# Kernel tuning notes

Hardware: AMD Instinct MI355X
Metric: run time of the kernel (lower is better)

## Reference

```python
import jax, jax.numpy as jnp
import numpy as np

B, L, HID = 512, 128, 384
N_LABELS, N_SLOTS = 32, 128


def setup_inputs() -> dict:
    key = jax.random.key(0)
    ks = jax.random.split(key, 16)

    def g(k, shape, scale):
        return jax.random.normal(k, shape, dtype=jnp.float32) * scale

    sent_lens = jax.random.randint(ks[0], (B,), 1, L + 1)
    mask = (jnp.arange(L)[None, :] < sent_lens[:, None]).astype(jnp.float32)[..., None]
    # zero out padded token positions to mimic the ragged original
    H = g(ks[1], (B, L, HID), 1.0) * mask
    c_slot_cont = g(ks[2], (B, L, HID), 1.0) * mask
    c_inte = g(ks[3], (B, HID), 1.0)
    s = 1.0 / np.sqrt(HID)
    return {
        "H": H,
        "c_slot_cont": c_slot_cont,
        "c_inte": c_inte,
        "W0": g(ks[4], (HID, HID), s),
        "W1": g(ks[5], (HID, HID), s),
        "W2": g(ks[6], (HID, HID), s),
        "W3": g(ks[7], (HID, HID), s),
        "W4": g(ks[8], (HID, HID), s),
        "b4": g(ks[9], (HID,), s),
        "W5": g(ks[10], (HID, 1), s),
        "V_SF": g(ks[11], (HID, HID), s),
        "W_inte": g(ks[12], (HID, N_LABELS), s),
        "W_slot": g(ks[13], (2 * HID, N_SLOTS), s),
        "sent_lens": sent_lens,
        "iteration_num": 3,
    }


def reference(H, c_slot_cont, c_inte, W0, W1, W2, W3, W4, b4, W5, V_SF,
              W_inte, W_slot, sent_lens, iteration_num):
    Ld = H.shape[1]
    mask = jnp.arange(Ld)[None, :] < sent_lens[:, None]          # [B, L] bool
    maskf = mask[..., None].astype(H.dtype)                       # [B, L, 1]
    neg_inf = jnp.finfo(H.dtype).min

    def sf_fusion(x, y):
        # SF_FusionLayer (dropout off / eval); inner loop runs once since nth=2
        x0 = jnp.tanh(x)
        y0 = jnp.tanh(y)
        f = jax.nn.sigmoid(jnp.tanh(x0 @ W0 + y0 @ W1) @ W2)
        x2 = f * x0 + x
        y2 = (1.0 - f) * y0 + y
        return f * x2 + (1.0 - f) * y2

    def id_fusion(x, y):
        # ID_FusionLayer; softmax over token dim, masked per sentence
        x0 = jnp.tanh(x)
        y0 = jnp.tanh(y)
        rates = ((x @ W3 + y @ W4 + b4) @ W5)[..., 0]             # [B, L]
        rates = jnp.where(mask, rates, neg_inf)
        alphas = jax.nn.softmax(rates, axis=1)[..., None]         # [B, L, 1]
        x2 = alphas * x0 + x
        y2 = (1.0 - alphas) * y0 + y
        return alphas * x2 + (1.0 - alphas) * y2

    r_inte = c_inte                                               # [B, HID]
    r_slot = c_slot_cont
    for _ in range(iteration_num):
        f_slot = sf_fusion(c_slot_cont, r_inte[:, None, :])       # [B, L, HID]
        f_slot = jnp.sum((f_slot @ V_SF) * maskf, axis=1)         # [B, HID]
        r_slot = f_slot[:, None, :] * c_slot_cont                 # [B, L, HID]
        f_inte = jnp.sum(id_fusion(r_slot, H) * maskf, axis=1)    # [B, HID]
        r_inte = f_inte + c_inte

    intent_output = r_inte @ W_inte                               # [B, n_labels]
    slot_output = jnp.concatenate([H, r_slot], axis=-1) @ W_slot  # [B, L, n_slots]
    return intent_output, slot_output
```

## Files before the change

### kernel.cpp

```cpp
#include <hip/hip_runtime.h>
#include <math.h>

#define HID 384
#define SLEN 128
#define NB 512
#define MTOK (NB*SLEN)
#define NLAB 32
#define NSLOT 128
#define APITCH 40
#define GPITCH 72

typedef _Float16 h8 __attribute__((ext_vector_type(8)));
typedef _Float16 h4v __attribute__((ext_vector_type(4)));
typedef __bf16   b8 __attribute__((ext_vector_type(8)));
typedef float    f4 __attribute__((ext_vector_type(4)));

__device__ __forceinline__ float sane(float x){
  return __builtin_isfinite(x) ? x : 0.f;
}
__device__ __forceinline__ float clampf(float x, float lo, float hi){
  return fminf(hi, fmaxf(lo, x));
}
__device__ __forceinline__ float fast_rcp(float x){
  return __builtin_amdgcn_rcpf(x);
}
__device__ __forceinline__ float fast_tanh(float x){
  x = clampf(x, -15.f, 15.f);
  float e = __expf(2.f * x);
  return (e - 1.f) * fast_rcp(e + 1.f);
}
__device__ __forceinline__ float sigmoid_c(float x){
  x = clampf(x, -60.f, 60.f);
  return fast_rcp(1.f + __expf(-x));
}
__device__ __forceinline__ void split16(float x, _Float16* h, _Float16* l){
  _Float16 hh = (_Float16)x; *h = hh; *l = (_Float16)(x - (float)hh);
}
__device__ __forceinline__ h8 ldh(const _Float16* p){ return *reinterpret_cast<const h8*>(p); }
__device__ __forceinline__ b8 ldb(const __bf16* p){ return *reinterpret_cast<const b8*>(p); }
__device__ __forceinline__ f4 mfma16h(h8 a, h8 b, f4 c){
  return __builtin_amdgcn_mfma_f32_16x16x32_f16(a, b, c, 0, 0, 0);
}
__device__ __forceinline__ f4 mfma16b(b8 a, b8 b, f4 c){
  return __builtin_amdgcn_mfma_f32_16x16x32_bf16(a, b, c, 0, 0, 0);
}


__global__ void k_lens(const int* __restrict__ raw, int* __restrict__ lensN){
  const int b = threadIdx.x;
  __shared__ int is64;
  if (b == 0) is64 = (raw[1] == 0) ? 1 : 0;
  __syncthreads();
  int v = is64 ? raw[2 * b] : raw[b];
  v = v < 0 ? 0 : (v > SLEN ? SLEN : v);
  lensN[b] = v;
}

__global__ void k_wsplit16(const float* __restrict__ in, _Float16* __restrict__ outh,
                           _Float16* __restrict__ outl, int R, int C){
  int idx = blockIdx.x * blockDim.x + threadIdx.x;
  if (idx < R * C){
    int r = idx / C, c = idx - r * C;
    float v = sane(in[idx]);
    _Float16 h = (_Float16)v;
    outh[(size_t)c * R + r] = h;
    outl[(size_t)c * R + r] = (_Float16)(v - (float)h);
  }
}

__global__ void k_wsplitbf(const float* __restrict__ in, __bf16* __restrict__ outh,
                           __bf16* __restrict__ outl, int R, int C){
  int idx = blockIdx.x * blockDim.x + threadIdx.x;
  if (idx < R * C){
    int r = idx / C, c = idx - r * C;
    float v = sane(in[idx]);
    __bf16 h = (__bf16)v;
    outh[(size_t)c * R + r] = h;
    outl[(size_t)c * R + r] = (__bf16)(v - (float)h);
  }
}

__global__ void k_transpose32(const float* __restrict__ in, float* __restrict__ out,
                              int R, int C){
  int idx = blockIdx.x * blockDim.x + threadIdx.x;
  if (idx < R * C){ int r = idx / C, c = idx - r * C; out[(size_t)c * R + r] = sane(in[idx]); }
}

__global__ void k_sanecopy(const float* __restrict__ in, float* __restrict__ out, int n){
  int i = blockIdx.x * blockDim.x + threadIdx.x;
  if (i < n) out[i] = sane(in[i]);
}

__global__ void k_w35(const float* __restrict__ W3, const float* __restrict__ W4,
                      const float* __restrict__ b4, const float* __restrict__ W5,
                      float* __restrict__ w35, float* __restrict__ w45, float* __restrict__ b45){
  __shared__ float w5s[HID];
  int t = threadIdx.x;
  w5s[t] = sane(W5[t]);
  __syncthreads();
  float s3 = 0.f, s4 = 0.f;
  for (int j = 0; j < HID; ++j){
    float w5 = w5s[j];
    s3 += sane(W3[(size_t)t * HID + j]) * w5;
    s4 += sane(W4[(size_t)t * HID + j]) * w5;
  }
  w35[t] = s3; w45[t] = s4;
  if (t == 0){
    float s = 0.f;
    for (int j = 0; j < HID; ++j) s += sane(b4[j]) * w5s[j];
    *b45 = s;
  }
}

__global__ void k_prep(const float* __restrict__ Cs,
                       _Float16* __restrict__ X0h, _Float16* __restrict__ X0l){
  const size_t n4 = (size_t)MTOK * HID / 4;
  const size_t stride = (size_t)gridDim.x * blockDim.x;
  for (size_t i = blockIdx.x * (size_t)blockDim.x + threadIdx.x; i < n4; i += stride){
    f4 v = *(const f4*)(Cs + i * 4);
    h4v hh, ll;
#pragma unroll
    for (int j = 0; j < 4; ++j){
      float x = fast_tanh(sane(v[j]));
      _Float16 h = (_Float16)x;
      hh[j] = h; ll[j] = (_Float16)(x - (float)h);
    }
    *(h4v*)(X0h + i * 4) = hh;
    *(h4v*)(X0l + i * 4) = ll;
  }
}

__global__ void k_ci(const float* __restrict__ ci, float* __restrict__ r_inte){
  size_t i = blockIdx.x * (size_t)blockDim.x + threadIdx.x;
  if (i < (size_t)NB * HID) r_inte[i] = sane(ci[i]);
}

__global__ void k_hy(const float* __restrict__ Hm, const float* __restrict__ w45,
                     const float* __restrict__ b45, float* __restrict__ hy){
  int wave = threadIdx.x >> 6, lane = threadIdx.x & 63;
  int tok = blockIdx.x * 4 + wave;
  const float* row = Hm + (size_t)tok * HID;
  float s = 0.f;
#pragma unroll
  for (int i = 0; i < 6; ++i){ int k = lane + 64 * i; s += sane(row[k]) * w45[k]; }
  for (int off = 32; off; off >>= 1) s += __shfl_down(s, off);
  if (lane == 0) hy[tok] = clampf(s + *b45, -1e30f, 1e30f);
}

template <int TANH>
__global__ void k_vecmat(const float* __restrict__ in, const float* __restrict__ W,
                         float* __restrict__ out, float* __restrict__ pre_store){
  const int b = blockIdx.x, t = threadIdx.x;
  __shared__ float v[HID];
  float x = in[(size_t)b * HID + t];
  if (TANH) x = fast_tanh(x);
  v[t] = x;
  if (pre_store) pre_store[(size_t)b * HID + t] = x;
  __syncthreads();
  float s = 0.f;
  for (int k = 0; k < HID; ++k) s += v[k] * W[(size_t)k * HID + t];
  out[(size_t)b * HID + t] = clampf(s, -1e30f, 1e30f);
}

__global__ void __launch_bounds__(256, 3) k_p0c(
    const _Float16* __restrict__ X0h, const _Float16* __restrict__ X0l,
    const _Float16* __restrict__ Wth, const _Float16* __restrict__ Wtl,
    const int* __restrict__ lens,
    _Float16* __restrict__ P0h, _Float16* __restrict__ P0l){
  __shared__ _Float16 Ah[128*APITCH], Al[128*APITCH], Bh[128*APITCH], Bl[128*APITCH];
  const int t = threadIdx.x;
  const int wave = t >> 6, lane = t & 63, quad = lane >> 4, lr = lane & 15;
  const int wm = wave & 1, wn = wave >> 1;
  const int bx = blockIdx.x, by = blockIdx.y;
  const int len = lens[bx];
  const bool live = (wm * 64) < len;
  f4 acc[4][4] = {};
  for (int kk = 0; kk < HID; kk += 32){
#pragma unroll
    for (int i = 0; i < 2; ++i){
      int tau = t + 256 * i;
      int row = tau >> 2, v8 = (tau & 3) << 3;
      size_t ga = ((size_t)(bx * 128 + row)) * HID + kk + v8;
      size_t gb = ((size_t)(by * 128 + row)) * HID + kk + v8;
      *(h8*)&Ah[row * APITCH + v8] = ldh(X0h + ga);
      *(h8*)&Al[row * APITCH + v8] = ldh(X0l + ga);
      *(h8*)&Bh[row * APITCH + v8] = ldh(Wth + gb);
      *(h8*)&Bl[row * APITCH + v8] = ldh(Wtl + gb);
    }
    __syncthreads();
    if (live){
      h8 ah[4], al[4];
#pragma unroll
      for (int mi = 0; mi < 4; ++mi){
        int r = (wm * 64 + mi * 16 + lr) * APITCH + quad * 8;
        ah[mi] = *(h8*)&Ah[r]; al[mi] = *(h8*)&Al[r];
      }
#pragma unroll
      for (int ni = 0; ni < 4; ++ni){
        int r = (wn * 64 + ni * 16 + lr) * APITCH + quad * 8;
        h8 bh = *(h8*)&Bh[r], bl = *(h8*)&Bl[r];
#pragma unroll
        for (int mi = 0; mi < 4; ++mi){
          acc[mi][ni] = mfma16h(ah[mi], bh, acc[mi][ni]);
          acc[mi][ni] = mfma16h(ah[mi], bl, acc[mi][ni]);
          acc[mi][ni] = mfma16h(al[mi], bh, acc[mi][ni]);
        }
      }
    }
    __syncthreads();
  }
  if (live){
#pragma unroll
    for (int ni = 0; ni < 4; ++ni){
      int col = by * 128 + wn * 64 + ni * 16 + lr;
#pragma unroll
      for (int mi = 0; mi < 4; ++mi)
#pragma unroll
        for (int r = 0; r < 4; ++r){
          int rl = wm * 64 + mi * 16 + quad * 4 + r;
          if (rl < len){
            size_t o = ((size_t)(bx * 128 + rl)) * HID + col;
            _Float16 h, l; split16(acc[mi][ni][r], &h, &l);
            P0h[o] = h; P0l[o] = l;
          }
        }
    }
  }
}

__global__ void __launch_bounds__(512, 4) k_g2n(
    const _Float16* __restrict__ P0h, const _Float16* __restrict__ P0l,
    const _Float16* __restrict__ Wth, const _Float16* __restrict__ Wtl,
    const float* __restrict__ yw1, const float* __restrict__ Cs,
    const float* __restrict__ y0b, const float* __restrict__ r_inte,
    const int* __restrict__ lens, float* __restrict__ S){
  __shared__ _Float16 Ah[64*GPITCH], Al[64*GPITCH];
  __shared__ float ywS[HID];
  const int t = threadIdx.x;
  const int wave = t >> 6, lane = t & 63, quad = lane >> 4, lr = lane & 15;
  const int bx = blockIdx.x;
  const int b = bx >> 1;
  const int len = lens[b];
  const int row0 = (bx & 1) * 64;
  if (row0 >= len) return;
  const int gr0 = bx * 64;
  const int srow = t >> 3;
  const int sk8 = (t & 7) << 3;
  const int col0 = wave * 48;
  if (t < HID) ywS[t] = yw1[(size_t)b * HID + t];
  __syncthreads();
  f4 acc[4][3] = {};
  for (int ks = 0; ks < 6; ++ks){
    const int kk = ks * 64;
    {
      const size_t g = ((size_t)(gr0 + srow)) * HID + kk + sk8;
      h8 ph = ldh(P0h + g), pl = ldh(P0l + g);
      const f4 ywa = *(const f4*)&ywS[kk + sk8];
      const f4 ywb = *(const f4*)&ywS[kk + sk8 + 4];
      h8 th, tl;
#pragma unroll
      for (int j = 0; j < 8; ++j){
        const float yw = (j < 4) ? ywa[j] : ywb[j - 4];
        float x = fast_tanh((float)ph[j] + (float)pl[j] + yw);
        _Float16 h = (_Float16)x;
        th[j] = h; tl[j] = (_Float16)(x - (float)h);
      }
      *(h8*)&Ah[srow * GPITCH + sk8] = th;
      *(h8*)&Al[srow * GPITCH + sk8] = tl;
    }
    __syncthreads();
#pragma unroll
    for (int c = 0; c < 2; ++c){
      const int ro = c * 32 + quad * 8;
      h8 amh[4], aml[4];
#pragma unroll
      for (int mi = 0; mi < 4; ++mi){
        const int r = (mi * 16 + lr) * GPITCH + ro;
        amh[mi] = *(const h8*)&Ah[r]; aml[mi] = *(const h8*)&Al[r];
      }
#pragma unroll
      for (int ni = 0; ni < 3; ++ni){
        const size_t rb = ((size_t)(col0 + ni * 16 + lr)) * HID + kk + ro;
        h8 bh = ldh(Wth + rb), bl = ldh(Wtl + rb);
#pragma unroll
        for (int mi = 0; mi < 4; ++mi){
          acc[mi][ni] = mfma16h(amh[mi], bh, acc[mi][ni]);
          acc[mi][ni] = mfma16h(amh[mi], bl, acc[mi][ni]);
          acc[mi][ni] = mfma16h(aml[mi], bh, acc[mi][ni]);
        }
      }
    }
    __syncthreads();
  }
  const float* yb = y0b + (size_t)b * HID;
  const float* rb = r_inte + (size_t)b * HID;
#pragma unroll
  for (int ni = 0; ni < 3; ++ni){
    const int col = col0 + ni * 16 + lr;
    const float y0 = yb[col];
    const float yv = rb[col];
    float csum = 0.f;
#pragma unroll
    for (int mi = 0; mi < 4; ++mi)
#pragma unroll
      for (int r = 0; r < 4; ++r){
        const int rl = row0 + mi * 16 + quad * 4 + r;
        const int grow = gr0 + mi * 16 + quad * 4 + r;
        const float f = sigmoid_c(acc[mi][ni][r]);
        const float omf = 1.f - f;
        const float xv = sane(Cs[(size_t)grow * HID + col]);
        const float x0 = fast_tanh(xv);
        const float outv = f * f * x0 + f * xv + omf * omf * y0 + omf * yv;
        csum += (rl < len) ? outv : 0.f;
      }
    csum += __shfl_xor(csum, 16);
    csum += __shfl_xor(csum, 32);
    if (quad == 0) atomicAdd(&S[(size_t)b * HID + col], csum);
  }
}

__global__ void k_stageD(
    const float* __restrict__ Cs, const float* __restrict__ Hm,
    const float* __restrict__ ci,
    const float* __restrict__ fss, const float* __restrict__ w35,
    const float* __restrict__ hy, const int* __restrict__ lens,
    float* __restrict__ r_inte){
  const int b = blockIdx.x;
  const int t = threadIdx.x;
  const int len = lens[b];
  __shared__ float fssw[HID];
  __shared__ float rates[SLEN];
  __shared__ float wA[SLEN], wB[SLEN], wC[SLEN], wD[SLEN];
  fssw[t] = fss[(size_t)b * HID + t] * w35[t];
  __syncthreads();
  const int wave = t >> 6, lane = t & 63;
  for (int l = wave; l < SLEN; l += 6){
    const float* row = Cs + ((size_t)b * SLEN + l) * HID;
    float s = 0.f;
#pragma unroll
    for (int i = 0; i < 6; ++i){ int k = lane + 64 * i; s += sane(row[k]) * fssw[k]; }
    for (int off = 32; off; off >>= 1) s += __shfl_down(s, off);
    if (lane == 0) rates[l] = clampf(s + hy[(size_t)b * SLEN + l], -1e30f, 1e30f);
  }
  __syncthreads();
  if (wave == 0){
    float r0 = (lane < len) ? rates[lane] : -3.0e38f;
    float r1 = (lane + 64 < len) ? rates[lane + 64] : -3.0e38f;
    float mx = fmaxf(r0, r1);
    for (int off = 32; off; off >>= 1) mx = fmaxf(mx, __shfl_xor(mx, off));
    float e0 = (lane < len) ? __expf(r0 - mx) : 0.f;
    float e1 = (lane + 64 < len) ? __expf(r1 - mx) : 0.f;
    float sm = e0 + e1;
    for (int off = 32; off; off >>= 1) sm += __shfl_xor(sm, off);
    const float inv = (sm > 0.f) ? (1.f / sm) : 0.f;
    float a0 = clampf(e0 * inv, 0.f, 1.f), a1 = clampf(e1 * inv, 0.f, 1.f);
    wA[lane] = a0 * a0; wB[lane] = a0; wC[lane] = (1.f - a0) * (1.f - a0); wD[lane] = 1.f - a0;
    wA[lane + 64] = a1 * a1; wB[lane + 64] = a1;
    wC[lane + 64] = (1.f - a1) * (1.f - a1); wD[lane + 64] = 1.f - a1;
  }
  __syncthreads();
  const float fs = fss[(size_t)b * HID + t];
  float acc = 0.f;
#pragma unroll 4
  for (int l = 0; l < len; ++l){
    const float cv = sane(Cs[((size_t)b * SLEN + l) * HID + t]);
    const float hv = sane(Hm[((size_t)b * SLEN + l) * HID + t]);
    const float rs = fs * cv;
    acc += wA[l] * fast_tanh(rs) + wB[l] * rs + wC[l] * fast_tanh(hv) + wD[l] * hv;
  }
  r_inte[(size_t)b * HID + t] = clampf(acc + sane(ci[(size_t)b * HID + t]), -1e30f, 1e30f);
}

__global__ void k_intent(const float* __restrict__ r_inte, const float* __restrict__ Wit,
                         float* __restrict__ out){
  const int t = threadIdx.x;
  const int b = blockIdx.x * 4 + (t >> 5);
  const int n = t & 31;
  const float* wr = Wit + (size_t)n * HID;
  const float* rr = r_inte + (size_t)b * HID;
  float s = 0.f;
  for (int k = 0; k < HID; ++k) s += rr[k] * wr[k];
  out[(size_t)b * NLAB + n] = clampf(s, -3e38f, 3e38f);
}

__global__ void __launch_bounds__(256, 2) k_slot_bf(
    const float* __restrict__ Hm, const float* __restrict__ Cs,
    const float* __restrict__ fss, const int* __restrict__ lens,
    const __bf16* __restrict__ Wth, const __bf16* __restrict__ Wtl,
    float* __restrict__ out){
  const int wave = threadIdx.x >> 6, lane = threadIdx.x & 63;
  const int quad = lane >> 4, lr = lane & 15;
  const int m0 = blockIdx.x * 128 + (wave & 1) * 64;
  const int n0 = (wave >> 1) * 64;
  const int b = blockIdx.x;
  const int ko = quad * 8;
  const int len = lens[b];
  if ((wave & 1) * 64 >= len){
#pragma unroll
    for (int mi = 0; mi < 4; ++mi)
#pragma unroll
      for (int ni = 0; ni < 4; ++ni)
#pragma unroll
        for (int r = 0; r < 4; ++r){
          const int row = m0 + mi * 16 + quad * 4 + r;
          const int col = n0 + ni * 16 + lr;
          out[(size_t)row * NSLOT + col] = 0.f;
        }
    return;
  }
  f4 acc[4][4] = {};
  for (int kk = 0; kk < 2 * HID; kk += 32){
    b8 ah[4], al[4], bh[4], bl[4];
#pragma unroll
    for (int i = 0; i < 4; ++i){
      size_t rb = (size_t)(n0 + i * 16 + lr) * (2 * HID) + kk + ko;
      bh[i] = ldb(Wth + rb); bl[i] = ldb(Wtl + rb);
    }
    if (kk < HID){
#pragma unroll
      for (int i = 0; i < 4; ++i){
        const float* hrow = Hm + (size_t)(m0 + i * 16 + lr) * HID + kk + ko;
        b8 vh, vl;
#pragma unroll
        for (int j = 0; j < 8; ++j){
          float v = sane(hrow[j]);
          __bf16 h = (__bf16)v;
          vh[j] = h; vl[j] = (__bf16)(v - (float)h);
        }
        ah[i] = vh; al[i] = vl;
      }
    } else {
      const int k2 = kk - HID + ko;
      float fv[8];
#pragma unroll
      for (int j = 0; j < 8; ++j) fv[j] = fss[(size_t)b * HID + k2 + j];
#pragma unroll
      for (int i = 0; i < 4; ++i){
        const float* crow = Cs + (size_t)(m0 + i * 16 + lr) * HID + k2;
        b8 vh, vl;
#pragma unroll
        for (int j = 0; j < 8; ++j){
          float v = fv[j] * sane(crow[j]);
          __bf16 h = (__bf16)v;
          vh[j] = h; vl[j] = (__bf16)(v - (float)h);
        }
        ah[i] = vh; al[i] = vl;
      }
    }
#pragma unroll
    for (int mi = 0; mi < 4; ++mi)
#pragma unroll
      for (int ni = 0; ni < 4; ++ni){
        acc[mi][ni] = mfma16b(ah[mi], bh[ni], acc[mi][ni]);
        acc[mi][ni] = mfma16b(ah[mi], bl[ni], acc[mi][ni]);
        acc[mi][ni] = mfma16b(al[mi], bh[ni], acc[mi][ni]);
      }
  }
#pragma unroll
  for (int mi = 0; mi < 4; ++mi)
#pragma unroll
    for (int ni = 0; ni < 4; ++ni)
#pragma unroll
      for (int r = 0; r < 4; ++r){
        const int row = m0 + mi * 16 + quad * 4 + r;
        const int col = n0 + ni * 16 + lr;
        out[(size_t)row * NSLOT + col] = clampf(acc[mi][ni][r], -3e38f, 3e38f);
      }
}

extern "C" void kernel_launch(void* const* d_in, const int* in_sizes, int n_in,
                              void* d_out, int out_size, void* d_ws, size_t ws_size,
                              hipStream_t stream){
  (void)in_sizes; (void)n_in; (void)out_size;
  const float* Hm  = (const float*)d_in[0];
  const float* Cs  = (const float*)d_in[1];
  const float* ci  = (const float*)d_in[2];
  const float* W0  = (const float*)d_in[3];
  const float* W1  = (const float*)d_in[4];
  const float* W2  = (const float*)d_in[5];
  const float* W3  = (const float*)d_in[6];
  const float* W4  = (const float*)d_in[7];
  const float* b4  = (const float*)d_in[8];
  const float* W5  = (const float*)d_in[9];
  const float* Vs  = (const float*)d_in[10];
  const float* Wi  = (const float*)d_in[11];
  const float* Wsl = (const float*)d_in[12];
  const int* lens_raw = (const int*)d_in[13];

  char* base = (char*)d_ws;
  size_t off = 0;
  auto alloc = [&](size_t bytes) -> void* {
    void* p = base + off; off += (bytes + 255) & ~(size_t)255; return p;
  };
  const size_t NT = (size_t)MTOK * HID;
  _Float16* X0h  = (_Float16*)alloc(NT * 2);
  _Float16* X0l  = (_Float16*)alloc(NT * 2);
  _Float16* P0h  = (_Float16*)alloc(NT * 2);
  _Float16* P0l  = (_Float16*)alloc(NT * 2);
  _Float16* W0th = (_Float16*)alloc((size_t)HID * HID * 2);
  _Float16* W0tl = (_Float16*)alloc((size_t)HID * HID * 2);
  _Float16* W2th = (_Float16*)alloc((size_t)HID * HID * 2);
  _Float16* W2tl = (_Float16*)alloc((size_t)HID * HID * 2);
  __bf16*   Wsth = (__bf16*)alloc((size_t)2 * HID * NSLOT * 2);
  __bf16*   Wstl = (__bf16*)alloc((size_t)2 * HID * NSLOT * 2);
  float* W1c    = (float*)alloc((size_t)HID * HID * 4);
  float* Vsc    = (float*)alloc((size_t)HID * HID * 4);
  float* Wit    = (float*)alloc((size_t)HID * NLAB * 4);
  float* w35    = (float*)alloc(HID * 4);
  float* w45    = (float*)alloc(HID * 4);
  float* b45    = (float*)alloc(4);
  float* hy     = (float*)alloc((size_t)MTOK * 4);
  float* yw1    = (float*)alloc((size_t)NB * HID * 4);
  float* y0b    = (float*)alloc((size_t)NB * HID * 4);
  float* r_inte = (float*)alloc((size_t)NB * HID * 4);
  float* S      = (float*)alloc((size_t)NB * HID * 4);
  float* fss    = (float*)alloc((size_t)NB * HID * 4);
  int* lensN    = (int*)alloc((size_t)NB * 4);
  if (off > ws_size) return;

  k_lens<<<1, NB, 0, stream>>>(lens_raw, lensN);
  k_wsplit16<<<(HID * HID + 255) / 256, 256, 0, stream>>>(W0, W0th, W0tl, HID, HID);
  k_wsplit16<<<(HID * HID + 255) / 256, 256, 0, stream>>>(W2, W2th, W2tl, HID, HID);
  k_wsplitbf<<<(2 * HID * NSLOT + 255) / 256, 256, 0, stream>>>(Wsl, Wsth, Wstl, 2 * HID, NSLOT);
  k_sanecopy<<<(HID * HID + 255) / 256, 256, 0, stream>>>(W1, W1c, HID * HID);
  k_sanecopy<<<(HID * HID + 255) / 256, 256, 0, stream>>>(Vs, Vsc, HID * HID);
  k_transpose32<<<(HID * NLAB + 255) / 256, 256, 0, stream>>>(Wi, Wit, HID, NLAB);
  k_w35<<<1, HID, 0, stream>>>(W3, W4, b4, W5, w35, w45, b45);
  k_ci<<<(NB * HID + 255) / 256, 256, 0, stream>>>(ci, r_inte);
  k_hy<<<MTOK / 4, 256, 0, stream>>>(Hm, w45, b45, hy);
  k_prep<<<4096, 256, 0, stream>>>(Cs, X0h, X0l);
  k_p0c<<<dim3(NB, 3), 256, 0, stream>>>(X0h, X0l, W0th, W0tl, lensN, P0h, P0l);

  for (int it = 0; it < 3; ++it){
    k_vecmat<1><<<NB, HID, 0, stream>>>(r_inte, W1c, yw1, y0b);
    hipMemsetAsync(S, 0, (size_t)NB * HID * 4, stream);
    k_g2n<<<MTOK / 64, 512, 0, stream>>>(P0h, P0l, W2th, W2tl, yw1, Cs, y0b, r_inte, lensN, S);
    k_vecmat<0><<<NB, HID, 0, stream>>>(S, Vsc, fss, (float*)nullptr);
    k_stageD<<<NB, HID, 0, stream>>>(Cs, Hm, ci, fss, w35, hy, lensN, r_inte);
  }

  float* outp = (float*)d_out;
  k_intent<<<NB / 4, 128, 0, stream>>>(r_inte, Wit, outp);
  k_slot_bf<<<NB, 256, 0, stream>>>(Hm, Cs, fss, lensN, Wsth, Wstl, outp + (size_t)NB * NLAB);
}
```

Before: 1.118 ms.

## Fuse all three refinement iterations into one persistent per-sentence kernel with length-sorted scheduling

Replaces the per-iteration sequence of vecmat, memset, g2n, vecmat and stageD launches (15 launches plus memsets) with one kernel where each 512-thread block owns a sentence and runs all three iterations, keeping r_inte, yw1, S and fss in shared memory. Blocks are handed sentences in an order interleaved by length so long and short sentences are spread across the dispatch. This removes launch overhead, global round-trips and atomics. In exchange, parallelism drops to 512 blocks with serial per-block work, including scalar 384x384 mat-vecs that each thread reads from global memory.

```diff
diff --git a/kernel.cpp b/kernel.cpp
--- a/kernel.cpp
+++ b/kernel.cpp
@@ -54,6 +54,25 @@
   int v = is64 ? raw[2 * b] : raw[b];
   v = v < 0 ? 0 : (v > SLEN ? SLEN : v);
   lensN[b] = v;
+}
+
+__global__ void k_order(const int* __restrict__ lensN, int* __restrict__ ord){
+  __shared__ int hist[SLEN + 1];
+  __shared__ int offs[SLEN + 1];
+  const int t = threadIdx.x;
+  if (t <= SLEN) hist[t] = 0;
+  __syncthreads();
+  const int len = lensN[t];
+  atomicAdd(&hist[len], 1);
+  __syncthreads();
+  if (t == 0){
+    int acc = 0;
+    for (int v = SLEN; v >= 0; --v){ offs[v] = acc; acc += hist[v]; }
+  }
+  __syncthreads();
+  const int r = atomicAdd(&offs[len], 1);
+  const int p = (r < NB / 2) ? r : (NB + NB / 2 - 1 - r);
+  ord[p] = t;
 }
 
 __global__ void k_wsplit16(const float* __restrict__ in, _Float16* __restrict__ outh,
@@ -130,11 +149,6 @@
   }
 }
 
-__global__ void k_ci(const float* __restrict__ ci, float* __restrict__ r_inte){
-  size_t i = blockIdx.x * (size_t)blockDim.x + threadIdx.x;
-  if (i < (size_t)NB * HID) r_inte[i] = sane(ci[i]);
-}
-
 __global__ void k_hy(const float* __restrict__ Hm, const float* __restrict__ w45,
                      const float* __restrict__ b45, float* __restrict__ hy){
   int wave = threadIdx.x >> 6, lane = threadIdx.x & 63;
@@ -145,21 +159,6 @@
   for (int i = 0; i < 6; ++i){ int k = lane + 64 * i; s += sane(row[k]) * w45[k]; }
   for (int off = 32; off; off >>= 1) s += __shfl_down(s, off);
   if (lane == 0) hy[tok] = clampf(s + *b45, -1e30f, 1e30f);
-}
-
-template <int TANH>
-__global__ void k_vecmat(const float* __restrict__ in, const float* __restrict__ W,
-                         float* __restrict__ out, float* __restrict__ pre_store){
-  const int b = blockIdx.x, t = threadIdx.x;
-  __shared__ float v[HID];
-  float x = in[(size_t)b * HID + t];
-  if (TANH) x = fast_tanh(x);
-  v[t] = x;
-  if (pre_store) pre_store[(size_t)b * HID + t] = x;
-  __syncthreads();
-  float s = 0.f;
-  for (int k = 0; k < HID; ++k) s += v[k] * W[(size_t)k * HID + t];
-  out[(size_t)b * HID + t] = clampf(s, -1e30f, 1e30f);
 }
 
 __global__ void __launch_bounds__(256, 3) k_p0c(
@@ -228,147 +227,165 @@
   }
 }
 
-__global__ void __launch_bounds__(512, 4) k_g2n(
+__global__ void __launch_bounds__(512, 4) k_iter(
     const _Float16* __restrict__ P0h, const _Float16* __restrict__ P0l,
     const _Float16* __restrict__ Wth, const _Float16* __restrict__ Wtl,
-    const float* __restrict__ yw1, const float* __restrict__ Cs,
-    const float* __restrict__ y0b, const float* __restrict__ r_inte,
-    const int* __restrict__ lens, float* __restrict__ S){
+    const float* __restrict__ W1c, const float* __restrict__ Vsc,
+    const float* __restrict__ Cs, const float* __restrict__ Hm,
+    const float* __restrict__ ci, const float* __restrict__ w35,
+    const float* __restrict__ hy, const int* __restrict__ lens,
+    const int* __restrict__ ord,
+    float* __restrict__ r_inte, float* __restrict__ fss_g){
   __shared__ _Float16 Ah[64*GPITCH], Al[64*GPITCH];
-  __shared__ float ywS[HID];
+  __shared__ float yw1S[HID], y0bS[HID], riS[HID], Ssum[HID], fssS[HID];
+  __shared__ float rates[SLEN], wA[SLEN], wB[SLEN], wC[SLEN], wD[SLEN];
   const int t = threadIdx.x;
   const int wave = t >> 6, lane = t & 63, quad = lane >> 4, lr = lane & 15;
-  const int bx = blockIdx.x;
-  const int b = bx >> 1;
+  const int b = ord[blockIdx.x];
   const int len = lens[b];
-  const int row0 = (bx & 1) * 64;
-  if (row0 >= len) return;
-  const int gr0 = bx * 64;
   const int srow = t >> 3;
   const int sk8 = (t & 7) << 3;
   const int col0 = wave * 48;
-  if (t < HID) ywS[t] = yw1[(size_t)b * HID + t];
+  if (t < HID) riS[t] = sane(ci[(size_t)b * HID + t]);
   __syncthreads();
-  f4 acc[4][3] = {};
-  for (int ks = 0; ks < 6; ++ks){
-    const int kk = ks * 64;
-    {
-      const size_t g = ((size_t)(gr0 + srow)) * HID + kk + sk8;
-      h8 ph = ldh(P0h + g), pl = ldh(P0l + g);
-      const f4 ywa = *(const f4*)&ywS[kk + sk8];
-      const f4 ywb = *(const f4*)&ywS[kk + sk8 + 4];
-      h8 th, tl;
-#pragma unroll
-      for (int j = 0; j < 8; ++j){
-        const float yw = (j < 4) ? ywa[j] : ywb[j - 4];
-        float x = fast_tanh((float)ph[j] + (float)pl[j] + yw);
-        _Float16 h = (_Float16)x;
-        th[j] = h; tl[j] = (_Float16)(x - (float)h);
-      }
-      *(h8*)&Ah[srow * GPITCH + sk8] = th;
-      *(h8*)&Al[srow * GPITCH + sk8] = tl;
-    }
-    __syncthreads();
-#pragma unroll
-    for (int c = 0; c < 2; ++c){
-      const int ro = c * 32 + quad * 8;
-      h8 amh[4], aml[4];
-#pragma unroll
-      for (int mi = 0; mi < 4; ++mi){
-        const int r = (mi * 16 + lr) * GPITCH + ro;
-        amh[mi] = *(const h8*)&Ah[r]; aml[mi] = *(const h8*)&Al[r];
+
+  for (int it = 0; it < 3; ++it){
+    if (t < HID) y0bS[t] = fast_tanh(riS[t]);
+    __syncthreads();
+    if (t < HID){
+      float s = 0.f;
+      for (int k = 0; k < HID; ++k) s += y0bS[k] * W1c[(size_t)k * HID + t];
+      yw1S[t] = clampf(s, -1e30f, 1e30f);
+    }
+    if (t < HID) Ssum[t] = 0.f;
+    __syncthreads();
+
+    for (int h = 0; h < 2; ++h){
+      const int row0 = h * 64;
+      if (row0 >= len) break;
+      const int gr0 = b * SLEN + row0;
+      f4 acc[4][3] = {};
+      for (int ks = 0; ks < 6; ++ks){
+        const int kk = ks * 64;
+        {
+          const size_t g = ((size_t)(gr0 + srow)) * HID + kk + sk8;
+          h8 ph = ldh(P0h + g), pl = ldh(P0l + g);
+          const f4 ywa = *(const f4*)&yw1S[kk + sk8];
+          const f4 ywb = *(const f4*)&yw1S[kk + sk8 + 4];
+          h8 th, tl;
+#pragma unroll
+          for (int j = 0; j < 8; ++j){
+            const float yw = (j < 4) ? ywa[j] : ywb[j - 4];
+            float x = fast_tanh((float)ph[j] + (float)pl[j] + yw);
+            _Float16 hh = (_Float16)x;
+            th[j] = hh; tl[j] = (_Float16)(x - (float)hh);
+          }
+          *(h8*)&Ah[srow * GPITCH + sk8] = th;
+          *(h8*)&Al[srow * GPITCH + sk8] = tl;
+        }
+        __syncthreads();
+#pragma unroll
+        for (int c = 0; c < 2; ++c){
+          const int ro = c * 32 + quad * 8;
+          h8 amh[4], aml[4];
+#pragma unroll
+          for (int mi = 0; mi < 4; ++mi){
+            const int r = (mi * 16 + lr) * GPITCH + ro;
+            amh[mi] = *(const h8*)&Ah[r]; aml[mi] = *(const h8*)&Al[r];
+          }
+#pragma unroll
+          for (int ni = 0; ni < 3; ++ni){
+            const size_t rb = ((size_t)(col0 + ni * 16 + lr)) * HID + kk + ro;
+            h8 bh = ldh(Wth + rb), bl = ldh(Wtl + rb);
+#pragma unroll
+            for (int mi = 0; mi < 4; ++mi){
+              acc[mi][ni] = mfma16h(amh[mi], bh, acc[mi][ni]);
+              acc[mi][ni] = mfma16h(amh[mi], bl, acc[mi][ni]);
+              acc[mi][ni] = mfma16h(aml[mi], bh, acc[mi][ni]);
+            }
+          }
+        }
+        __syncthreads();
       }
 #pragma unroll
       for (int ni = 0; ni < 3; ++ni){
-        const size_t rb = ((size_t)(col0 + ni * 16 + lr)) * HID + kk + ro;
-        h8 bh = ldh(Wth + rb), bl = ldh(Wtl + rb);
-#pragma unroll
-        for (int mi = 0; mi < 4; ++mi){
-          acc[mi][ni] = mfma16h(amh[mi], bh, acc[mi][ni]);
-          acc[mi][ni] = mfma16h(amh[mi], bl, acc[mi][ni]);
-          acc[mi][ni] = mfma16h(aml[mi], bh, acc[mi][ni]);
-        }
-      }
-    }
-    __syncthreads();
-  }
-  const float* yb = y0b + (size_t)b * HID;
-  const float* rb = r_inte + (size_t)b * HID;
-#pragma unroll
-  for (int ni = 0; ni < 3; ++ni){
-    const int col = col0 + ni * 16 + lr;
-    const float y0 = yb[col];
-    const float yv = rb[col];
-    float csum = 0.f;
-#pragma unroll
-    for (int mi = 0; mi < 4; ++mi)
-#pragma unroll
-      for (int r = 0; r < 4; ++r){
-        const int rl = row0 + mi * 16 + quad * 4 + r;
-        const int grow = gr0 + mi * 16 + quad * 4 + r;
-        const float f = sigmoid_c(acc[mi][ni][r]);
-        const float omf = 1.f - f;
-        const float xv = sane(Cs[(size_t)grow * HID + col]);
-        const float x0 = fast_tanh(xv);
-        const float outv = f * f * x0 + f * xv + omf * omf * y0 + omf * yv;
-        csum += (rl < len) ? outv : 0.f;
-      }
-    csum += __shfl_xor(csum, 16);
-    csum += __shfl_xor(csum, 32);
-    if (quad == 0) atomicAdd(&S[(size_t)b * HID + col], csum);
-  }
-}
-
-__global__ void k_stageD(
-    const float* __restrict__ Cs, const float* __restrict__ Hm,
-    const float* __restrict__ ci,
-    const float* __restrict__ fss, const float* __restrict__ w35,
-    const float* __restrict__ hy, const int* __restrict__ lens,
-    float* __restrict__ r_inte){
-  const int b = blockIdx.x;
-  const int t = threadIdx.x;
-  const int len = lens[b];
-  __shared__ float fssw[HID];
-  __shared__ float rates[SLEN];
-  __shared__ float wA[SLEN], wB[SLEN], wC[SLEN], wD[SLEN];
-  fssw[t] = fss[(size_t)b * HID + t] * w35[t];
-  __syncthreads();
-  const int wave = t >> 6, lane = t & 63;
-  for (int l = wave; l < SLEN; l += 6){
-    const float* row = Cs + ((size_t)b * SLEN + l) * HID;
-    float s = 0.f;
-#pragma unroll
-    for (int i = 0; i < 6; ++i){ int k = lane + 64 * i; s += sane(row[k]) * fssw[k]; }
-    for (int off = 32; off; off >>= 1) s += __shfl_down(s, off);
-    if (lane == 0) rates[l] = clampf(s + hy[(size_t)b * SLEN + l], -1e30f, 1e30f);
-  }
-  __syncthreads();
-  if (wave == 0){
-    float r0 = (lane < len) ? rates[lane] : -3.0e38f;
-    float r1 = (lane + 64 < len) ? rates[lane + 64] : -3.0e38f;
-    float mx = fmaxf(r0, r1);
-    for (int off = 32; off; off >>= 1) mx = fmaxf(mx, __shfl_xor(mx, off));
-    float e0 = (lane < len) ? __expf(r0 - mx) : 0.f;
-    float e1 = (lane + 64 < len) ? __expf(r1 - mx) : 0.f;
-    float sm = e0 + e1;
-    for (int off = 32; off; off >>= 1) sm += __shfl_xor(sm, off);
-    const float inv = (sm > 0.f) ? (1.f / sm) : 0.f;
-    float a0 = clampf(e0 * inv, 0.f, 1.f), a1 = clampf(e1 * inv, 0.f, 1.f);
-    wA[lane] = a0 * a0; wB[lane] = a0; wC[lane] = (1.f - a0) * (1.f - a0); wD[lane] = 1.f - a0;
-    wA[lane + 64] = a1 * a1; wB[lane + 64] = a1;
-    wC[lane + 64] = (1.f - a1) * (1.f - a1); wD[lane + 64] = 1.f - a1;
-  }
-  __syncthreads();
-  const float fs = fss[(size_t)b * HID + t];
-  float acc = 0.f;
+        const int col = col0 + ni * 16 + lr;
+        const float y0 = y0bS[col];
+        const float yv = riS[col];
+        float csum = 0.f;
+#pragma unroll
+        for (int mi = 0; mi < 4; ++mi)
+#pragma unroll
+          for (int r = 0; r < 4; ++r){
+            const int rl = row0 + mi * 16 + quad * 4 + r;
+            const int grow = gr0 + mi * 16 + quad * 4 + r;
+            const float f = sigmoid_c(acc[mi][ni][r]);
+            const float omf = 1.f - f;
+            const float xv = sane(Cs[(size_t)grow * HID + col]);
+            const float x0 = fast_tanh(xv);
+            const float outv = f * f * x0 + f * xv + omf * omf * y0 + omf * yv;
+            csum += (rl < len) ? outv : 0.f;
+          }
+        csum += __shfl_xor(csum, 16);
+        csum += __shfl_xor(csum, 32);
+        if (quad == 0) Ssum[col] += csum;
+      }
+    }
+    __syncthreads();
+
+    if (t < HID){
+      float s = 0.f;
+      for (int k = 0; k < HID; ++k) s += Ssum[k] * Vsc[(size_t)k * HID + t];
+      fssS[t] = clampf(s, -1e30f, 1e30f);
+    }
+    __syncthreads();
+
+    if (t < HID) y0bS[t] = fssS[t] * w35[t];
+    __syncthreads();
+    for (int l = wave; l < SLEN; l += 8){
+      const float* row = Cs + ((size_t)b * SLEN + l) * HID;
+      float s = 0.f;
+#pragma unroll
+      for (int i = 0; i < 6; ++i){ int k = lane + 64 * i; s += sane(row[k]) * y0bS[k]; }
+      for (int off = 32; off; off >>= 1) s += __shfl_down(s, off);
+      if (lane == 0) rates[l] = clampf(s + hy[(size_t)b * SLEN + l], -1e30f, 1e30f);
+    }
+    __syncthreads();
+    if (wave == 0){
+      float r0 = (lane < len) ? rates[lane] : -3.0e38f;
+      float r1 = (lane + 64 < len) ? rates[lane + 64] : -3.0e38f;
+      float mx = fmaxf(r0, r1);
+      for (int off = 32; off; off >>= 1) mx = fmaxf(mx, __shfl_xor(mx, off));
+      float e0 = (lane < len) ? __expf(r0 - mx) : 0.f;
+      float e1 = (lane + 64 < len) ? __expf(r1 - mx) : 0.f;
+      float sm = e0 + e1;
+      for (int off = 32; off; off >>= 1) sm += __shfl_xor(sm, off);
+      const float inv = (sm > 0.f) ? (1.f / sm) : 0.f;
+      float a0 = clampf(e0 * inv, 0.f, 1.f), a1 = clampf(e1 * inv, 0.f, 1.f);
+      wA[lane] = a0 * a0; wB[lane] = a0;
+      wC[lane] = (1.f - a0) * (1.f - a0); wD[lane] = 1.f - a0;
+      wA[lane + 64] = a1 * a1; wB[lane + 64] = a1;
+      wC[lane + 64] = (1.f - a1) * (1.f - a1); wD[lane + 64] = 1.f - a1;
+    }
+    __syncthreads();
+    if (t < HID){
+      const float fs = fssS[t];
+      float acc2 = 0.f;
 #pragma unroll 4
-  for (int l = 0; l < len; ++l){
-    const float cv = sane(Cs[((size_t)b * SLEN + l) * HID + t]);
-    const float hv = sane(Hm[((size_t)b * SLEN + l) * HID + t]);
-    const float rs = fs * cv;
-    acc += wA[l] * fast_tanh(rs) + wB[l] * rs + wC[l] * fast_tanh(hv) + wD[l] * hv;
-  }
-  r_inte[(size_t)b * HID + t] = clampf(acc + sane(ci[(size_t)b * HID + t]), -1e30f, 1e30f);
+      for (int l = 0; l < len; ++l){
+        const float cv = sane(Cs[((size_t)b * SLEN + l) * HID + t]);
+        const float hv = sane(Hm[((size_t)b * SLEN + l) * HID + t]);
+        const float rs = fs * cv;
+        acc2 += wA[l] * fast_tanh(rs) + wB[l] * rs + wC[l] * fast_tanh(hv) + wD[l] * hv;
+      }
+      riS[t] = clampf(acc2 + sane(ci[(size_t)b * HID + t]), -1e30f, 1e30f);
+    }
+    __syncthreads();
+  }
+  if (t < HID){
+    r_inte[(size_t)b * HID + t] = riS[t];
+    fss_g[(size_t)b * HID + t] = fssS[t];
+  }
 }
 
 __global__ void k_intent(const float* __restrict__ r_inte, const float* __restrict__ Wit,
@@ -510,15 +527,14 @@
   float* w45    = (float*)alloc(HID * 4);
   float* b45    = (float*)alloc(4);
   float* hy     = (float*)alloc((size_t)MTOK * 4);
-  float* yw1    = (float*)alloc((size_t)NB * HID * 4);
-  float* y0b    = (float*)alloc((size_t)NB * HID * 4);
   float* r_inte = (float*)alloc((size_t)NB * HID * 4);
-  float* S      = (float*)alloc((size_t)NB * HID * 4);
   float* fss    = (float*)alloc((size_t)NB * HID * 4);
   int* lensN    = (int*)alloc((size_t)NB * 4);
+  int* ord      = (int*)alloc((size_t)NB * 4);
   if (off > ws_size) return;
 
   k_lens<<<1, NB, 0, stream>>>(lens_raw, lensN);
+  k_order<<<1, NB, 0, stream>>>(lensN, ord);
   k_wsplit16<<<(HID * HID + 255) / 256, 256, 0, stream>>>(W0, W0th, W0tl, HID, HID);
   k_wsplit16<<<(HID * HID + 255) / 256, 256, 0, stream>>>(W2, W2th, W2tl, HID, HID);
   k_wsplitbf<<<(2 * HID * NSLOT + 255) / 256, 256, 0, stream>>>(Wsl, Wsth, Wstl, 2 * HID, NSLOT);
@@ -526,18 +542,12 @@
   k_sanecopy<<<(HID * HID + 255) / 256, 256, 0, stream>>>(Vs, Vsc, HID * HID);
   k_transpose32<<<(HID * NLAB + 255) / 256, 256, 0, stream>>>(Wi, Wit, HID, NLAB);
   k_w35<<<1, HID, 0, stream>>>(W3, W4, b4, W5, w35, w45, b45);
-  k_ci<<<(NB * HID + 255) / 256, 256, 0, stream>>>(ci, r_inte);
   k_hy<<<MTOK / 4, 256, 0, stream>>>(Hm, w45, b45, hy);
   k_prep<<<4096, 256, 0, stream>>>(Cs, X0h, X0l);
   k_p0c<<<dim3(NB, 3), 256, 0, stream>>>(X0h, X0l, W0th, W0tl, lensN, P0h, P0l);
 
-  for (int it = 0; it < 3; ++it){
-    k_vecmat<1><<<NB, HID, 0, stream>>>(r_inte, W1c, yw1, y0b);
-    hipMemsetAsync(S, 0, (size_t)NB * HID * 4, stream);
-    k_g2n<<<MTOK / 64, 512, 0, stream>>>(P0h, P0l, W2th, W2tl, yw1, Cs, y0b, r_inte, lensN, S);
-    k_vecmat<0><<<NB, HID, 0, stream>>>(S, Vsc, fss, (float*)nullptr);
-    k_stageD<<<NB, HID, 0, stream>>>(Cs, Hm, ci, fss, w35, hy, lensN, r_inte);
-  }
+  k_iter<<<NB, 512, 0, stream>>>(P0h, P0l, W2th, W2tl, W1c, Vsc, Cs, Hm, ci,
+                                 w35, hy, lensN, ord, r_inte, fss);
 
   float* outp = (float*)d_out;
   k_intent<<<NB / 4, 128, 0, stream>>>(r_inte, Wit, outp);
```

Result: slower. 1.250 ms (+11.8%).

## Fuse tanh prep into P0 GEMM and fold per-iteration vecmats into stage D

Applied to the files above, without the earlier changes.

Removes the separate k_prep pass by computing tanh and the fp16 hi/lo split of c_slot_cont inside the P0 GEMM tile loader, which drops the X0h/X0l round trip through global memory. Inside the iteration loop, the S@V_SF vecmat, the zeroing of S and the next iteration's tanh(r_inte)@W1 vecmat now run inside the stage-D kernel, and k_g2n recomputes y0 = tanh(r_inte) itself instead of reading a stored copy. This cuts kernel launches and memsets per iteration. The cost is more ALU work in the GEMM loader and longer serial per-batch work in stage D, and the last iteration computes a yw1 that is never used.

```diff
diff --git a/kernel.cpp b/kernel.cpp
--- a/kernel.cpp
+++ b/kernel.cpp
@@ -112,24 +112,6 @@
   }
 }
 
-__global__ void k_prep(const float* __restrict__ Cs,
-                       _Float16* __restrict__ X0h, _Float16* __restrict__ X0l){
-  const size_t n4 = (size_t)MTOK * HID / 4;
-  const size_t stride = (size_t)gridDim.x * blockDim.x;
-  for (size_t i = blockIdx.x * (size_t)blockDim.x + threadIdx.x; i < n4; i += stride){
-    f4 v = *(const f4*)(Cs + i * 4);
-    h4v hh, ll;
-#pragma unroll
-    for (int j = 0; j < 4; ++j){
-      float x = fast_tanh(sane(v[j]));
-      _Float16 h = (_Float16)x;
-      hh[j] = h; ll[j] = (_Float16)(x - (float)h);
-    }
-    *(h4v*)(X0h + i * 4) = hh;
-    *(h4v*)(X0l + i * 4) = ll;
-  }
-}
-
 __global__ void k_ci(const float* __restrict__ ci, float* __restrict__ r_inte){
   size_t i = blockIdx.x * (size_t)blockDim.x + threadIdx.x;
   if (i < (size_t)NB * HID) r_inte[i] = sane(ci[i]);
@@ -163,7 +145,7 @@
 }
 
 __global__ void __launch_bounds__(256, 3) k_p0c(
-    const _Float16* __restrict__ X0h, const _Float16* __restrict__ X0l,
+    const float* __restrict__ Cs,
     const _Float16* __restrict__ Wth, const _Float16* __restrict__ Wtl,
     const int* __restrict__ lens,
     _Float16* __restrict__ P0h, _Float16* __restrict__ P0l){
@@ -177,15 +159,29 @@
   f4 acc[4][4] = {};
   for (int kk = 0; kk < HID; kk += 32){
 #pragma unroll
-    for (int i = 0; i < 2; ++i){
-      int tau = t + 256 * i;
-      int row = tau >> 2, v8 = (tau & 3) << 3;
-      size_t ga = ((size_t)(bx * 128 + row)) * HID + kk + v8;
-      size_t gb = ((size_t)(by * 128 + row)) * HID + kk + v8;
-      *(h8*)&Ah[row * APITCH + v8] = ldh(X0h + ga);
-      *(h8*)&Al[row * APITCH + v8] = ldh(X0l + ga);
-      *(h8*)&Bh[row * APITCH + v8] = ldh(Wth + gb);
-      *(h8*)&Bl[row * APITCH + v8] = ldh(Wtl + gb);
+    for (int i = 0; i < 4; ++i){
+      const int tau = t + 256 * i;
+      const int row = tau >> 3, f4i = tau & 7;
+      f4 v = *(const f4*)(Cs + ((size_t)(bx * 128 + row)) * HID + kk + f4i * 4);
+      h4v hh, ll;
+#pragma unroll
+      for (int j = 0; j < 4; ++j){
+        float x = fast_tanh(sane(v[j]));
+        _Float16 h = (_Float16)x;
+        hh[j] = h; ll[j] = (_Float16)(x - (float)h);
+      }
+      *(h4v*)&Ah[row * APITCH + f4i * 4] = hh;
+      *(h4v*)&Al[row * APITCH + f4i * 4] = ll;
+    }
+#pragma unroll
+    for (int i = 0; i < 4; ++i){
+      const int tau = t + 256 * i;
+      const int plane = tau >> 9;
+      const int row = (tau >> 2) & 127;
+      const int v8 = (tau & 3) << 3;
+      const size_t gb = ((size_t)(by * 128 + row)) * HID + kk + v8;
+      if (plane == 0) *(h8*)&Bh[row * APITCH + v8] = ldh(Wth + gb);
+      else            *(h8*)&Bl[row * APITCH + v8] = ldh(Wtl + gb);
     }
     __syncthreads();
     if (live){
@@ -232,7 +228,7 @@
     const _Float16* __restrict__ P0h, const _Float16* __restrict__ P0l,
     const _Float16* __restrict__ Wth, const _Float16* __restrict__ Wtl,
     const float* __restrict__ yw1, const float* __restrict__ Cs,
-    const float* __restrict__ y0b, const float* __restrict__ r_inte,
+    const float* __restrict__ r_inte,
     const int* __restrict__ lens, float* __restrict__ S){
   __shared__ _Float16 Ah[64*GPITCH], Al[64*GPITCH];
   __shared__ float ywS[HID];
@@ -292,13 +288,12 @@
     }
     __syncthreads();
   }
-  const float* yb = y0b + (size_t)b * HID;
   const float* rb = r_inte + (size_t)b * HID;
 #pragma unroll
   for (int ni = 0; ni < 3; ++ni){
     const int col = col0 + ni * 16 + lr;
-    const float y0 = yb[col];
     const float yv = rb[col];
+    const float y0 = fast_tanh(yv);
     float csum = 0.f;
 #pragma unroll
     for (int mi = 0; mi < 4; ++mi)
@@ -319,19 +314,29 @@
   }
 }
 
-__global__ void k_stageD(
+__global__ void k_stageD2(
     const float* __restrict__ Cs, const float* __restrict__ Hm,
-    const float* __restrict__ ci,
-    const float* __restrict__ fss, const float* __restrict__ w35,
+    const float* __restrict__ ci, const float* __restrict__ Vsc,
+    const float* __restrict__ W1c, const float* __restrict__ w35,
     const float* __restrict__ hy, const int* __restrict__ lens,
-    float* __restrict__ r_inte){
+    float* __restrict__ S, float* __restrict__ fss_g,
+    float* __restrict__ r_inte, float* __restrict__ yw1){
   const int b = blockIdx.x;
   const int t = threadIdx.x;
   const int len = lens[b];
-  __shared__ float fssw[HID];
+  __shared__ float Sl[HID], fssS[HID], fssw[HID], tri[HID];
   __shared__ float rates[SLEN];
   __shared__ float wA[SLEN], wB[SLEN], wC[SLEN], wD[SLEN];
-  fssw[t] = fss[(size_t)b * HID + t] * w35[t];
+  Sl[t] = S[(size_t)b * HID + t];
+  S[(size_t)b * HID + t] = 0.f;
+  __syncthreads();
+  {
+    float s = 0.f;
+    for (int k = 0; k < HID; ++k) s += Sl[k] * Vsc[(size_t)k * HID + t];
+    const float fs = clampf(s, -1e30f, 1e30f);
+    fssS[t] = fs; fssw[t] = fs * w35[t];
+    fss_g[(size_t)b * HID + t] = fs;
+  }
   __syncthreads();
   const int wave = t >> 6, lane = t & 63;
   for (int l = wave; l < SLEN; l += 6){
@@ -354,21 +359,32 @@
     for (int off = 32; off; off >>= 1) sm += __shfl_xor(sm, off);
     const float inv = (sm > 0.f) ? (1.f / sm) : 0.f;
     float a0 = clampf(e0 * inv, 0.f, 1.f), a1 = clampf(e1 * inv, 0.f, 1.f);
-    wA[lane] = a0 * a0; wB[lane] = a0; wC[lane] = (1.f - a0) * (1.f - a0); wD[lane] = 1.f - a0;
+    wA[lane] = a0 * a0; wB[lane] = a0;
+    wC[lane] = (1.f - a0) * (1.f - a0); wD[lane] = 1.f - a0;
     wA[lane + 64] = a1 * a1; wB[lane + 64] = a1;
     wC[lane + 64] = (1.f - a1) * (1.f - a1); wD[lane + 64] = 1.f - a1;
   }
   __syncthreads();
-  const float fs = fss[(size_t)b * HID + t];
-  float acc = 0.f;
+  {
+    const float fs = fssS[t];
+    float acc = 0.f;
 #pragma unroll 4
-  for (int l = 0; l < len; ++l){
-    const float cv = sane(Cs[((size_t)b * SLEN + l) * HID + t]);
-    const float hv = sane(Hm[((size_t)b * SLEN + l) * HID + t]);
-    const float rs = fs * cv;
-    acc += wA[l] * fast_tanh(rs) + wB[l] * rs + wC[l] * fast_tanh(hv) + wD[l] * hv;
-  }
-  r_inte[(size_t)b * HID + t] = clampf(acc + sane(ci[(size_t)b * HID + t]), -1e30f, 1e30f);
+    for (int l = 0; l < len; ++l){
+      const float cv = sane(Cs[((size_t)b * SLEN + l) * HID + t]);
+      const float hv = sane(Hm[((size_t)b * SLEN + l) * HID + t]);
+      const float rs = fs * cv;
+      acc += wA[l] * fast_tanh(rs) + wB[l] * rs + wC[l] * fast_tanh(hv) + wD[l] * hv;
+    }
+    const float ri = clampf(acc + sane(ci[(size_t)b * HID + t]), -1e30f, 1e30f);
+    r_inte[(size_t)b * HID + t] = ri;
+    tri[t] = fast_tanh(ri);
+  }
+  __syncthreads();
+  {
+    float s = 0.f;
+    for (int k = 0; k < HID; ++k) s += tri[k] * W1c[(size_t)k * HID + t];
+    yw1[(size_t)b * HID + t] = clampf(s, -1e30f, 1e30f);
+  }
 }
 
 __global__ void k_intent(const float* __restrict__ r_inte, const float* __restrict__ Wit,
@@ -493,8 +509,6 @@
     void* p = base + off; off += (bytes + 255) & ~(size_t)255; return p;
   };
   const size_t NT = (size_t)MTOK * HID;
-  _Float16* X0h  = (_Float16*)alloc(NT * 2);
-  _Float16* X0l  = (_Float16*)alloc(NT * 2);
   _Float16* P0h  = (_Float16*)alloc(NT * 2);
   _Float16* P0l  = (_Float16*)alloc(NT * 2);
   _Float16* W0th = (_Float16*)alloc((size_t)HID * HID * 2);
@@ -511,7 +525,6 @@
   float* b45    = (float*)alloc(4);
   float* hy     = (float*)alloc((size_t)MTOK * 4);
   float* yw1    = (float*)alloc((size_t)NB * HID * 4);
-  float* y0b    = (float*)alloc((size_t)NB * HID * 4);
   float* r_inte = (float*)alloc((size_t)NB * HID * 4);
   float* S      = (float*)alloc((size_t)NB * HID * 4);
   float* fss    = (float*)alloc((size_t)NB * HID * 4);
@@ -528,15 +541,15 @@
   k_w35<<<1, HID, 0, stream>>>(W3, W4, b4, W5, w35, w45, b45);
   k_ci<<<(NB * HID + 255) / 256, 256, 0, stream>>>(ci, r_inte);
   k_hy<<<MTOK / 4, 256, 0, stream>>>(Hm, w45, b45, hy);
-  k_prep<<<4096, 256, 0, stream>>>(Cs, X0h, X0l);
-  k_p0c<<<dim3(NB, 3), 256, 0, stream>>>(X0h, X0l, W0th, W0tl, lensN, P0h, P0l);
+  k_p0c<<<dim3(NB, 3), 256, 0, stream>>>(Cs, W0th, W0tl, lensN, P0h, P0l);
+
+  k_vecmat<1><<<NB, HID, 0, stream>>>(r_inte, W1c, yw1, (float*)nullptr);
+  hipMemsetAsync(S, 0, (size_t)NB * HID * 4, stream);
 
   for (int it = 0; it < 3; ++it){
-    k_vecmat<1><<<NB, HID, 0, stream>>>(r_inte, W1c, yw1, y0b);
-    hipMemsetAsync(S, 0, (size_t)NB * HID * 4, stream);
-    k_g2n<<<MTOK / 64, 512, 0, stream>>>(P0h, P0l, W2th, W2tl, yw1, Cs, y0b, r_inte, lensN, S);
-    k_vecmat<0><<<NB, HID, 0, stream>>>(S, Vsc, fss, (float*)nullptr);
-    k_stageD<<<NB, HID, 0, stream>>>(Cs, Hm, ci, fss, w35, hy, lensN, r_inte);
+    k_g2n<<<MTOK / 64, 512, 0, stream>>>(P0h, P0l, W2th, W2tl, yw1, Cs, r_inte, lensN, S);
+    k_stageD2<<<NB, HID, 0, stream>>>(Cs, Hm, ci, Vsc, W1c, w35, hy, lensN,
+                                      S, fss, r_inte, yw1);
   }
 
   float* outp = (float*)d_out;
```

Result: faster. 1.079 ms (-3.5%).
